# Kernel tuning notes

Measured on AMD Instinct MI355X. Metric: run time of the kernel, lower is better.

The kernel has to match this reference:

```python
import jax, jax.numpy as jnp
import numpy as np

D_MODEL = 512
N_HEADS = 8
D_K = D_MODEL // N_HEADS
D_DTW = 21


def setup_inputs() -> dict:
    key = jax.random.key(0)
    ks = jax.random.split(key, 16)
    bs, S = 16, 512
    def lin(k, fan_in, shape):
        return jax.random.uniform(k, shape, jnp.float32, -1.0, 1.0) / np.sqrt(fan_in)
    return {
        "Q": jax.random.normal(ks[0], (bs, S, D_MODEL), jnp.float32),
        "K": jax.random.normal(ks[1], (bs, S, D_MODEL), jnp.float32),
        "V": jax.random.normal(ks[2], (bs, S, D_MODEL), jnp.float32),
        "G": jax.random.normal(ks[3], (bs, S, D_MODEL), jnp.float32),
        "dtw_cost": jax.random.uniform(ks[4], (bs, D_DTW, S, S), jnp.float32),
        "Wq": lin(ks[5], D_MODEL, (D_MODEL, D_MODEL)), "bq": lin(ks[6], D_MODEL, (D_MODEL,)),
        "Wk": lin(ks[7], D_MODEL, (D_MODEL, D_MODEL)), "bk": lin(ks[8], D_MODEL, (D_MODEL,)),
        "Wv": lin(ks[9], D_MODEL, (D_MODEL, D_MODEL)), "bv": lin(ks[10], D_MODEL, (D_MODEL,)),
        "Wd": lin(ks[11], D_DTW, (N_HEADS, D_DTW)), "bd": lin(ks[12], D_DTW, (N_HEADS,)),
        "Wo": lin(ks[13], D_MODEL, (D_MODEL, D_MODEL)), "bo": lin(ks[14], D_MODEL, (D_MODEL,)),
    }


def reference(Q, K, V, G, dtw_cost, Wq, bq, Wk, bk, Wv, bv, Wd, bd, Wo, bo):
    bs, S, _ = Q.shape
    # QKV projections, split into heads: [bs, H, S, dk]
    def proj(x, W, b):
        y = x @ W.T + b
        return y.reshape(bs, S, N_HEADS, D_K).transpose(0, 2, 1, 3)
    q = proj(Q, Wq, bq)
    k = proj(K, Wk, bk)
    v = proj(V, Wv, bv)
    # scaled dot-product scores [bs, H, S, S]
    scores = jnp.einsum("bhqd,bhkd->bhqk", q, k) / np.sqrt(D_K).astype(np.float32)
    # DTW-cost bias: linear over the cost-channel dim (21 -> H), added per head
    bias = jnp.einsum("bcqk,hc->bhqk", dtw_cost, Wd) + bd[None, :, None, None]
    attn = jax.nn.softmax(scores + bias, axis=-1)
    out = jnp.einsum("bhqk,bhkd->bhqd", attn, v)  # [bs, H, S, dk]
    concat = out.transpose(0, 2, 1, 3).reshape(bs, S, D_MODEL)
    output = concat @ Wo.T + bo
    return (output, attn)
```

## Files before the change

kernel.cpp:

```cpp
#include <hip/hip_runtime.h>
#include <hip/hip_bf16.h>
#include <cstddef>
#include <cstdint>

#define BS   16
#define SLEN 512
#define DM   512
#define NH   8
#define DK   64
#define DC   21

typedef __attribute__((ext_vector_type(8))) short short8;
typedef __attribute__((ext_vector_type(4))) float f32x4;
typedef __attribute__((ext_vector_type(8))) _Float16 h16x8;
typedef _Float16 h16x4a __attribute__((ext_vector_type(4), may_alias));

__device__ inline unsigned pack_bf16(float a, float b) {
    unsigned ua = __builtin_bit_cast(unsigned, a);
    unsigned ub = __builtin_bit_cast(unsigned, b);
    ua = (ua + 0x7fffu + ((ua >> 16) & 1u)) >> 16;
    ub = (ub + 0x7fffu + ((ub >> 16) & 1u)) >> 16;
    return ua | (ub << 16);
}
__device__ inline unsigned cvt2(float a, float b) { return pack_bf16(a, b); }
__device__ inline ushort bf16_1(float a) { return (ushort)(pack_bf16(a, 0.f) & 0xffffu); }
__device__ inline unsigned pk_f16(float a, float b) {
    return __builtin_bit_cast(unsigned, __builtin_amdgcn_cvt_pkrtz(a, b));
}

__device__ __host__ inline size_t bias_chunk_base(int bh, int q16) {
    return 2 * (((size_t)bh * SLEN + (size_t)q16) * SLEN);
}

template<int MODE>
__global__ __launch_bounds__(256) void gemm_bf16(
    const void* __restrict__ Xv, const float* __restrict__ W,
    const float* __restrict__ bias, void* __restrict__ outv)
{
    __shared__ alignas(16) ushort Atile[64 * 64];
    __shared__ alignas(16) ushort Btile[128 * 64];

    const float*  Xf = (const float*)Xv;
    const ushort* Xb = (const ushort*)Xv;

    const int tid = threadIdx.x;
    const int wave = tid >> 6, lane = tid & 63;
    const int lq = lane & 15, lg = lane >> 4;
    const int wr = wave >> 1, wc = wave & 1;
    const int m0 = blockIdx.x * 64;
    const int n0 = blockIdx.y * 128;

    f32x4 acc[2][4];
#pragma unroll
    for (int i = 0; i < 2; ++i)
#pragma unroll
        for (int j = 0; j < 4; ++j) acc[i][j] = (f32x4){0.f, 0.f, 0.f, 0.f};

    float4 pa[2][2], pb[4][2];
    uint4  qa[2];

#define LOAD_A(K0)                                                              \
    if (MODE == 3) {                                                            \
        _Pragma("unroll")                                                       \
        for (int i = 0; i < 2; ++i) {                                           \
            const int P = tid + 256 * i;                                        \
            const int row = P >> 3, sl = P & 7;                                 \
            qa[i] = *(const uint4*)&Xb[(size_t)(m0 + row) * 512 + (K0) + sl * 8]; \
        }                                                                       \
    } else {                                                                    \
        _Pragma("unroll")                                                       \
        for (int i = 0; i < 2; ++i) {                                           \
            const int P = tid + 256 * i;                                        \
            const int row = P >> 3, cp = P & 7;                                 \
            const float4* s = (const float4*)&Xf[(size_t)(m0 + row) * 512 + (K0) + cp * 8]; \
            pa[i][0] = s[0]; pa[i][1] = s[1];                                   \
        }                                                                       \
    }
#define LOAD_B(K0)                                                              \
    _Pragma("unroll")                                                           \
    for (int i = 0; i < 4; ++i) {                                               \
        const int P = tid + 256 * i;                                            \
        const int row = P >> 3, cp = P & 7;                                     \
        const float4* s = (const float4*)&W[(size_t)(n0 + row) * 512 + (K0) + cp * 8]; \
        pb[i][0] = s[0]; pb[i][1] = s[1];                                       \
    }

    LOAD_A(0)
    LOAD_B(0)

    for (int it = 0; it < 8; ++it) {
        __syncthreads();
        if (MODE == 3) {
#pragma unroll
            for (int i = 0; i < 2; ++i) {
                const int P = tid + 256 * i;
                const int row = P >> 3, sl = P & 7;
                *(uint4*)((char*)Atile + row * 128 + 16 * (sl ^ (row & 7))) = qa[i];
            }
        } else {
#pragma unroll
            for (int i = 0; i < 2; ++i) {
                const int P = tid + 256 * i;
                const int row = P >> 3, cp = P & 7;
                uint4 w;
                w.x = cvt2(pa[i][0].x, pa[i][0].y);
                w.y = cvt2(pa[i][0].z, pa[i][0].w);
                w.z = cvt2(pa[i][1].x, pa[i][1].y);
                w.w = cvt2(pa[i][1].z, pa[i][1].w);
                *(uint4*)((char*)Atile + row * 128 + 16 * (cp ^ (row & 7))) = w;
            }
        }
#pragma unroll
        for (int i = 0; i < 4; ++i) {
            const int P = tid + 256 * i;
            const int row = P >> 3, cp = P & 7;
            uint4 w;
            w.x = cvt2(pb[i][0].x, pb[i][0].y);
            w.y = cvt2(pb[i][0].z, pb[i][0].w);
            w.z = cvt2(pb[i][1].x, pb[i][1].y);
            w.w = cvt2(pb[i][1].z, pb[i][1].w);
            *(uint4*)((char*)Btile + row * 128 + 16 * (cp ^ (row & 7))) = w;
        }
        __syncthreads();

        if (it < 7) {
            const int kn = (it + 1) * 64;
            LOAD_A(kn)
            LOAD_B(kn)
        }

        short8 af[2][2], bfr[4][2];
#pragma unroll
        for (int mi = 0; mi < 2; ++mi)
#pragma unroll
            for (int kh = 0; kh < 2; ++kh) {
                const int row = wr * 32 + mi * 16 + lq;
                af[mi][kh] = *(const short8*)((const char*)Atile + row * 128 +
                                              16 * ((kh * 4 + lg) ^ (row & 7)));
            }
#pragma unroll
        for (int ni = 0; ni < 4; ++ni)
#pragma unroll
            for (int kh = 0; kh < 2; ++kh) {
                const int row = wc * 64 + ni * 16 + lq;
                bfr[ni][kh] = *(const short8*)((const char*)Btile + row * 128 +
                                               16 * ((kh * 4 + lg) ^ (row & 7)));
            }
        __builtin_amdgcn_s_setprio(1);
#pragma unroll
        for (int kh = 0; kh < 2; ++kh)
#pragma unroll
            for (int mi = 0; mi < 2; ++mi)
#pragma unroll
                for (int ni = 0; ni < 4; ++ni)
                    acc[mi][ni] = __builtin_amdgcn_mfma_f32_16x16x32_bf16(
                        af[mi][kh], bfr[ni][kh], acc[mi][ni], 0, 0, 0);
        __builtin_amdgcn_s_setprio(0);
    }
#undef LOAD_A
#undef LOAD_B

    if (MODE == 3) {
        float* out = (float*)outv;
#pragma unroll
        for (int mi = 0; mi < 2; ++mi) {
            const int mb = m0 + wr * 32 + mi * 16 + lg * 4;
#pragma unroll
            for (int ni = 0; ni < 4; ++ni) {
                const int n = n0 + wc * 64 + ni * 16 + lq;
                const float bb = bias[n];
#pragma unroll
                for (int r = 0; r < 4; ++r)
                    out[(size_t)(mb + r) * 512 + n] = acc[mi][ni][r] + bb;
            }
        }
    } else if (MODE == 1) {
        ushort* out = (ushort*)outv;
#pragma unroll
        for (int mi = 0; mi < 2; ++mi) {
            const int mb = m0 + wr * 32 + mi * 16 + lg * 4;
#pragma unroll
            for (int ni = 0; ni < 4; ++ni) {
                const int n = n0 + wc * 64 + ni * 16 + lq;
                const int h = n >> 6, d = n & 63;
                const float bb = bias[n];
#pragma unroll
                for (int r = 0; r < 4; ++r) {
                    const int m = mb + r;
                    const int bidx = m >> 9, s = m & 511;
                    out[((size_t)(bidx * NH + h) * SLEN + s) * DK + d] =
                        bf16_1(acc[mi][ni][r] + bb);
                }
            }
        }
    } else {
        ushort* out = (ushort*)outv;
#pragma unroll
        for (int mi = 0; mi < 2; ++mi) {
            const int mb = m0 + wr * 32 + mi * 16 + lg * 4;
            const int bidx = mb >> 9, s0 = mb & 511;
#pragma unroll
            for (int ni = 0; ni < 4; ++ni) {
                const int n = n0 + wc * 64 + ni * 16 + lq;
                const int h = n >> 6, d = n & 63;
                const float bb = bias[n];
                uint2 pk;
                pk.x = pk_f16(acc[mi][ni][0] + bb, acc[mi][ni][1] + bb);
                pk.y = pk_f16(acc[mi][ni][2] + bb, acc[mi][ni][3] + bb);
                *(uint2*)&out[((size_t)(bidx * NH + h) * DK + d) * SLEN + s0] = pk;
            }
        }
    }
}

__global__ __launch_bounds__(512) void bias_kernel(
    const float* __restrict__ dtw, const float* __restrict__ Wd,
    const float* __restrict__ bd, _Float16* __restrict__ bias16)
{
    __shared__ float wdl[NH * DC];
    __shared__ float bdl[NH];
    const int k = threadIdx.x;
    const int q = blockIdx.x;
    const int b = blockIdx.y;
    if (k < NH * DC) wdl[k] = Wd[k];
    if (k < NH) bdl[k] = bd[k];
    __syncthreads();

    float acc[NH];
#pragma unroll
    for (int h = 0; h < NH; ++h) acc[h] = bdl[h];

    const float* p = dtw + ((size_t)b * DC * SLEN + q) * SLEN + k;
#pragma unroll
    for (int c = 0; c < DC; ++c) {
        const float x = p[(size_t)c * SLEN * SLEN];
#pragma unroll
        for (int h = 0; h < NH; ++h) acc[h] += x * wdl[h * DC + c];
    }
    const int q16 = q & ~15, ql = q & 15;
    const size_t seg = 1024 * (size_t)ql + 64 * (size_t)(k >> 5) + (k & 31);
#pragma unroll
    for (int h = 0; h < NH; ++h) {
        const size_t base = bias_chunk_base(b * NH + h, q16);
        bias16[base + seg] = (_Float16)acc[h];
    }
}

__global__ __launch_bounds__(256, 3) void attn_mfma(
    const ushort* __restrict__ qb, const ushort* __restrict__ kb,
    const ushort* __restrict__ vt, float* __restrict__ attn,
    ushort* __restrict__ concat)
{
    __shared__ alignas(16) ushort Pbuf[4][2][16][32];

    const int tid = threadIdx.x;
    const int wave = tid >> 6;
    const int lane = tid & 63;
    const int lq = lane & 15;
    const int lg = lane >> 4;

    const unsigned l = blockIdx.x;
    const int g  = (int)((l & 7) + 8 * (l >> 6));
    const int qt = (int)((l >> 3) & 7);
    const int h = g & 7, b = g >> 3;
    const int bh = b * NH + h;
    const int q0 = qt * 64 + wave * 16;

    const ushort* qptr = qb + ((size_t)bh * SLEN + q0) * DK;
    const ushort* kptr = kb + (size_t)bh * SLEN * DK;
    const ushort* vptr = vt + (size_t)bh * DK * SLEN;
    float* attn_b = attn + ((size_t)bh * SLEN + q0) * SLEN;
    const _Float16* bias_row =
        (const _Float16*)attn + bias_chunk_base(bh, q0) + 1024 * (size_t)lq;

    const short8 qf0 = *(const short8*)&qptr[(size_t)lq * DK + lg * 8];
    const short8 qf1 = *(const short8*)&qptr[(size_t)lq * DK + lg * 8 + 32];

    float sum = 0.f;
#pragma unroll 8
    for (int kt = 0; kt < 32; ++kt) {
        const short8 a0 = *(const short8*)&kptr[(size_t)(kt * 16 + lq) * DK + lg * 8];
        const short8 a1 = *(const short8*)&kptr[(size_t)(kt * 16 + lq) * DK + lg * 8 + 32];
        f32x4 c = {0.f, 0.f, 0.f, 0.f};
        c = __builtin_amdgcn_mfma_f32_16x16x32_bf16(a0, qf0, c, 0, 0, 0);
        c = __builtin_amdgcn_mfma_f32_16x16x32_bf16(a1, qf1, c, 0, 0, 0);
        const h16x4a b4 = *(const h16x4a*)&bias_row[64 * (kt >> 1) + 16 * (kt & 1) + 4 * lg];
        const float s0 = c[0] * 0.125f + (float)b4[0];
        const float s1 = c[1] * 0.125f + (float)b4[1];
        const float s2 = c[2] * 0.125f + (float)b4[2];
        const float s3 = c[3] * 0.125f + (float)b4[3];
        sum += (__expf(s0) + __expf(s1)) + (__expf(s2) + __expf(s3));
    }
    sum += __shfl_xor(sum, 16);
    sum += __shfl_xor(sum, 32);
    const float inv = 1.0f / sum;

    f32x4 oacc[4] = {{0.f,0.f,0.f,0.f},{0.f,0.f,0.f,0.f},{0.f,0.f,0.f,0.f},{0.f,0.f,0.f,0.f}};

#pragma unroll 2
    for (int c2 = 15; c2 >= 0; --c2) {
        f32x4 ev[2];
#pragma unroll
        for (int t = 0; t < 2; ++t) {
            const int kt = 2 * c2 + t;
            const short8 a0 = *(const short8*)&kptr[(size_t)(kt * 16 + lq) * DK + lg * 8];
            const short8 a1 = *(const short8*)&kptr[(size_t)(kt * 16 + lq) * DK + lg * 8 + 32];
            f32x4 c = {0.f, 0.f, 0.f, 0.f};
            c = __builtin_amdgcn_mfma_f32_16x16x32_bf16(a0, qf0, c, 0, 0, 0);
            c = __builtin_amdgcn_mfma_f32_16x16x32_bf16(a1, qf1, c, 0, 0, 0);
            const h16x4a b4 = *(const h16x4a*)&bias_row[64 * c2 + 16 * t + 4 * lg];
            ev[t][0] = __expf(c[0] * 0.125f + (float)b4[0]);
            ev[t][1] = __expf(c[1] * 0.125f + (float)b4[1]);
            ev[t][2] = __expf(c[2] * 0.125f + (float)b4[2]);
            ev[t][3] = __expf(c[3] * 0.125f + (float)b4[3]);
        }
#pragma unroll
        for (int t = 0; t < 2; ++t)
            *(f32x4*)&attn_b[(size_t)lq * SLEN + (2 * c2 + t) * 16 + lg * 4] = ev[t] * inv;

        char* pb = (char*)&Pbuf[wave][c2 & 1][0][0];
#pragma unroll
        for (int t = 0; t < 2; ++t) {
            uint2 pk;
            pk.x = pk_f16(ev[t][0], ev[t][1]);
            pk.y = pk_f16(ev[t][2], ev[t][3]);
            const int slot = (t * 2 + (lg >> 1)) ^ (lq & 3);
            *(uint2*)(pb + lq * 64 + slot * 16 + (lg & 1) * 8) = pk;
        }
        asm volatile("s_waitcnt lgkmcnt(0)" ::: "memory");

        const h16x8 pa = *(const h16x8*)(pb + lq * 64 + (lg ^ (lq & 3)) * 16);
        __builtin_amdgcn_s_setprio(1);
#pragma unroll
        for (int dt = 0; dt < 4; ++dt) {
            const h16x8 vb8 = *(const h16x8*)&vptr[(size_t)(dt * 16 + lq) * SLEN + c2 * 32 + lg * 8];
            oacc[dt] = __builtin_amdgcn_mfma_f32_16x16x32_f16(pa, vb8, oacc[dt], 0, 0, 0);
        }
        __builtin_amdgcn_s_setprio(0);
    }

    ushort* cbase = concat + ((size_t)(b * SLEN + q0)) * DM + h * 64;
#pragma unroll
    for (int r = 0; r < 4; ++r) {
        const float iv = __shfl(inv, lg * 4 + r);
#pragma unroll
        for (int dt = 0; dt < 4; ++dt) {
            cbase[(size_t)(lg * 4 + r) * DM + dt * 16 + lq] = bf16_1(oacc[dt][r] * iv);
        }
    }
}

extern "C" void kernel_launch(void* const* d_in, const int* in_sizes, int n_in,
                              void* d_out, int out_size, void* d_ws, size_t ws_size,
                              hipStream_t stream)
{
    const float* Q   = (const float*)d_in[0];
    const float* K   = (const float*)d_in[1];
    const float* V   = (const float*)d_in[2];
    const float* dtw = (const float*)d_in[4];
    const float* Wq  = (const float*)d_in[5];
    const float* bq  = (const float*)d_in[6];
    const float* Wk  = (const float*)d_in[7];
    const float* bk  = (const float*)d_in[8];
    const float* Wv  = (const float*)d_in[9];
    const float* bv  = (const float*)d_in[10];
    const float* Wd  = (const float*)d_in[11];
    const float* bd  = (const float*)d_in[12];
    const float* Wo  = (const float*)d_in[13];
    const float* bo  = (const float*)d_in[14];

    float* out  = (float*)d_out;
    float* attn = out + (size_t)BS * SLEN * DM;
    _Float16* bias16 = (_Float16*)attn;

    const size_t PHS = (size_t)BS * NH * SLEN * DK;
    ushort* qb = (ushort*)d_ws;
    ushort* kb = qb + PHS;
    ushort* vt = kb + PHS;
    ushort* cb = vt + PHS;

    const dim3 gemm_grid(128, 4);

    gemm_bf16<1><<<gemm_grid, 256, 0, stream>>>(Q, Wq, bq, qb);
    gemm_bf16<1><<<gemm_grid, 256, 0, stream>>>(K, Wk, bk, kb);
    gemm_bf16<2><<<gemm_grid, 256, 0, stream>>>(V, Wv, bv, vt);

    bias_kernel<<<dim3(SLEN, BS), 512, 0, stream>>>(dtw, Wd, bd, bias16);

    attn_mfma<<<dim3(1024), 256, 0, stream>>>(qb, kb, vt, attn, cb);

    gemm_bf16<3><<<gemm_grid, 256, 0, stream>>>(cb, Wo, bo, out);
}
```

Before: 299.6 us.

## Single-pass attention with deferred normalization; merge QKV GEMMs into one launch

The attention kernel no longer runs a separate QK^T and exp pass just to get the softmax denominator. It now computes scores once, writes unnormalized exp values to the attn output and accumulates the row sum. It then rescales the stored attn rows by 1/sum in a final read-modify-write loop. This removes half the score MFMAs and exps, but adds an extra read and write of the large attn tensor. The three QKV projection GEMMs are merged into one launch using blockIdx.z, the output GEMM gets its own kernel, the bias layout is regrouped to 32-wide chunks, and attention occupancy is raised to 4 blocks per CU.

```diff
diff --git a/kernel.cpp b/kernel.cpp
--- a/kernel.cpp
+++ b/kernel.cpp
@@ -32,16 +32,22 @@
     return 2 * (((size_t)bh * SLEN + (size_t)q16) * SLEN);
 }
 
-template<int MODE>
-__global__ __launch_bounds__(256) void gemm_bf16(
-    const void* __restrict__ Xv, const float* __restrict__ W,
-    const float* __restrict__ bias, void* __restrict__ outv)
+__global__ __launch_bounds__(256) void gemm_qkv(
+    const float* __restrict__ Q, const float* __restrict__ K,
+    const float* __restrict__ V,
+    const float* __restrict__ Wq, const float* __restrict__ Wk,
+    const float* __restrict__ Wv,
+    const float* __restrict__ bq, const float* __restrict__ bk,
+    const float* __restrict__ bv,
+    ushort* __restrict__ qb, ushort* __restrict__ kb, ushort* __restrict__ vt)
 {
     __shared__ alignas(16) ushort Atile[64 * 64];
     __shared__ alignas(16) ushort Btile[128 * 64];
 
-    const float*  Xf = (const float*)Xv;
-    const ushort* Xb = (const ushort*)Xv;
+    const int z = blockIdx.z;
+    const float* X    = (z == 0) ? Q  : (z == 1) ? K  : V;
+    const float* W    = (z == 0) ? Wq : (z == 1) ? Wk : Wv;
+    const float* bias = (z == 0) ? bq : (z == 1) ? bk : bv;
 
     const int tid = threadIdx.x;
     const int wave = tid >> 6, lane = tid & 63;
@@ -57,24 +63,14 @@
         for (int j = 0; j < 4; ++j) acc[i][j] = (f32x4){0.f, 0.f, 0.f, 0.f};
 
     float4 pa[2][2], pb[4][2];
-    uint4  qa[2];
 
 #define LOAD_A(K0)                                                              \
-    if (MODE == 3) {                                                            \
-        _Pragma("unroll")                                                       \
-        for (int i = 0; i < 2; ++i) {                                           \
-            const int P = tid + 256 * i;                                        \
-            const int row = P >> 3, sl = P & 7;                                 \
-            qa[i] = *(const uint4*)&Xb[(size_t)(m0 + row) * 512 + (K0) + sl * 8]; \
-        }                                                                       \
-    } else {                                                                    \
-        _Pragma("unroll")                                                       \
-        for (int i = 0; i < 2; ++i) {                                           \
-            const int P = tid + 256 * i;                                        \
-            const int row = P >> 3, cp = P & 7;                                 \
-            const float4* s = (const float4*)&Xf[(size_t)(m0 + row) * 512 + (K0) + cp * 8]; \
-            pa[i][0] = s[0]; pa[i][1] = s[1];                                   \
-        }                                                                       \
+    _Pragma("unroll")                                                           \
+    for (int i = 0; i < 2; ++i) {                                               \
+        const int P = tid + 256 * i;                                            \
+        const int row = P >> 3, cp = P & 7;                                     \
+        const float4* s = (const float4*)&X[(size_t)(m0 + row) * 512 + (K0) + cp * 8]; \
+        pa[i][0] = s[0]; pa[i][1] = s[1];                                       \
     }
 #define LOAD_B(K0)                                                              \
     _Pragma("unroll")                                                           \
@@ -90,25 +86,16 @@
 
     for (int it = 0; it < 8; ++it) {
         __syncthreads();
-        if (MODE == 3) {
-#pragma unroll
-            for (int i = 0; i < 2; ++i) {
-                const int P = tid + 256 * i;
-                const int row = P >> 3, sl = P & 7;
-                *(uint4*)((char*)Atile + row * 128 + 16 * (sl ^ (row & 7))) = qa[i];
-            }
-        } else {
-#pragma unroll
-            for (int i = 0; i < 2; ++i) {
-                const int P = tid + 256 * i;
-                const int row = P >> 3, cp = P & 7;
-                uint4 w;
-                w.x = cvt2(pa[i][0].x, pa[i][0].y);
-                w.y = cvt2(pa[i][0].z, pa[i][0].w);
-                w.z = cvt2(pa[i][1].x, pa[i][1].y);
-                w.w = cvt2(pa[i][1].z, pa[i][1].w);
-                *(uint4*)((char*)Atile + row * 128 + 16 * (cp ^ (row & 7))) = w;
-            }
+#pragma unroll
+        for (int i = 0; i < 2; ++i) {
+            const int P = tid + 256 * i;
+            const int row = P >> 3, cp = P & 7;
+            uint4 w;
+            w.x = cvt2(pa[i][0].x, pa[i][0].y);
+            w.y = cvt2(pa[i][0].z, pa[i][0].w);
+            w.z = cvt2(pa[i][1].x, pa[i][1].y);
+            w.w = cvt2(pa[i][1].z, pa[i][1].w);
+            *(uint4*)((char*)Atile + row * 128 + 16 * (cp ^ (row & 7))) = w;
         }
 #pragma unroll
         for (int i = 0; i < 4; ++i) {
@@ -160,22 +147,8 @@
 #undef LOAD_A
 #undef LOAD_B
 
-    if (MODE == 3) {
-        float* out = (float*)outv;
-#pragma unroll
-        for (int mi = 0; mi < 2; ++mi) {
-            const int mb = m0 + wr * 32 + mi * 16 + lg * 4;
-#pragma unroll
-            for (int ni = 0; ni < 4; ++ni) {
-                const int n = n0 + wc * 64 + ni * 16 + lq;
-                const float bb = bias[n];
-#pragma unroll
-                for (int r = 0; r < 4; ++r)
-                    out[(size_t)(mb + r) * 512 + n] = acc[mi][ni][r] + bb;
-            }
-        }
-    } else if (MODE == 1) {
-        ushort* out = (ushort*)outv;
+    if (z < 2) {
+        ushort* out = (z == 0) ? qb : kb;
 #pragma unroll
         for (int mi = 0; mi < 2; ++mi) {
             const int mb = m0 + wr * 32 + mi * 16 + lg * 4;
@@ -194,7 +167,6 @@
             }
         }
     } else {
-        ushort* out = (ushort*)outv;
 #pragma unroll
         for (int mi = 0; mi < 2; ++mi) {
             const int mb = m0 + wr * 32 + mi * 16 + lg * 4;
@@ -207,8 +179,122 @@
                 uint2 pk;
                 pk.x = pk_f16(acc[mi][ni][0] + bb, acc[mi][ni][1] + bb);
                 pk.y = pk_f16(acc[mi][ni][2] + bb, acc[mi][ni][3] + bb);
-                *(uint2*)&out[((size_t)(bidx * NH + h) * DK + d) * SLEN + s0] = pk;
-            }
+                *(uint2*)&vt[((size_t)(bidx * NH + h) * DK + d) * SLEN + s0] = pk;
+            }
+        }
+    }
+}
+
+__global__ __launch_bounds__(256) void gemm_out(
+    const ushort* __restrict__ Xb, const float* __restrict__ W,
+    const float* __restrict__ bias, float* __restrict__ out)
+{
+    __shared__ alignas(16) ushort Atile[64 * 64];
+    __shared__ alignas(16) ushort Btile[128 * 64];
+
+    const int tid = threadIdx.x;
+    const int wave = tid >> 6, lane = tid & 63;
+    const int lq = lane & 15, lg = lane >> 4;
+    const int wr = wave >> 1, wc = wave & 1;
+    const int m0 = blockIdx.x * 64;
+    const int n0 = blockIdx.y * 128;
+
+    f32x4 acc[2][4];
+#pragma unroll
+    for (int i = 0; i < 2; ++i)
+#pragma unroll
+        for (int j = 0; j < 4; ++j) acc[i][j] = (f32x4){0.f, 0.f, 0.f, 0.f};
+
+    uint4  qa[2];
+    float4 pb[4][2];
+
+#define LOAD_A(K0)                                                              \
+    _Pragma("unroll")                                                           \
+    for (int i = 0; i < 2; ++i) {                                               \
+        const int P = tid + 256 * i;                                            \
+        const int row = P >> 3, sl = P & 7;                                     \
+        qa[i] = *(const uint4*)&Xb[(size_t)(m0 + row) * 512 + (K0) + sl * 8];   \
+    }
+#define LOAD_B(K0)                                                              \
+    _Pragma("unroll")                                                           \
+    for (int i = 0; i < 4; ++i) {                                               \
+        const int P = tid + 256 * i;                                            \
+        const int row = P >> 3, cp = P & 7;                                     \
+        const float4* s = (const float4*)&W[(size_t)(n0 + row) * 512 + (K0) + cp * 8]; \
+        pb[i][0] = s[0]; pb[i][1] = s[1];                                       \
+    }
+
+    LOAD_A(0)
+    LOAD_B(0)
+
+    for (int it = 0; it < 8; ++it) {
+        __syncthreads();
+#pragma unroll
+        for (int i = 0; i < 2; ++i) {
+            const int P = tid + 256 * i;
+            const int row = P >> 3, sl = P & 7;
+            *(uint4*)((char*)Atile + row * 128 + 16 * (sl ^ (row & 7))) = qa[i];
+        }
+#pragma unroll
+        for (int i = 0; i < 4; ++i) {
+            const int P = tid + 256 * i;
+            const int row = P >> 3, cp = P & 7;
+            uint4 w;
+            w.x = cvt2(pb[i][0].x, pb[i][0].y);
+            w.y = cvt2(pb[i][0].z, pb[i][0].w);
+            w.z = cvt2(pb[i][1].x, pb[i][1].y);
+            w.w = cvt2(pb[i][1].z, pb[i][1].w);
+            *(uint4*)((char*)Btile + row * 128 + 16 * (cp ^ (row & 7))) = w;
+        }
+        __syncthreads();
+
+        if (it < 7) {
+            const int kn = (it + 1) * 64;
+            LOAD_A(kn)
+            LOAD_B(kn)
+        }
+
+        short8 af[2][2], bfr[4][2];
+#pragma unroll
+        for (int mi = 0; mi < 2; ++mi)
+#pragma unroll
+            for (int kh = 0; kh < 2; ++kh) {
+                const int row = wr * 32 + mi * 16 + lq;
+                af[mi][kh] = *(const short8*)((const char*)Atile + row * 128 +
+                                              16 * ((kh * 4 + lg) ^ (row & 7)));
+            }
+#pragma unroll
+        for (int ni = 0; ni < 4; ++ni)
+#pragma unroll
+            for (int kh = 0; kh < 2; ++kh) {
+                const int row = wc * 64 + ni * 16 + lq;
+                bfr[ni][kh] = *(const short8*)((const char*)Btile + row * 128 +
+                                               16 * ((kh * 4 + lg) ^ (row & 7)));
+            }
+        __builtin_amdgcn_s_setprio(1);
+#pragma unroll
+        for (int kh = 0; kh < 2; ++kh)
+#pragma unroll
+            for (int mi = 0; mi < 2; ++mi)
+#pragma unroll
+                for (int ni = 0; ni < 4; ++ni)
+                    acc[mi][ni] = __builtin_amdgcn_mfma_f32_16x16x32_bf16(
+                        af[mi][kh], bfr[ni][kh], acc[mi][ni], 0, 0, 0);
+        __builtin_amdgcn_s_setprio(0);
+    }
+#undef LOAD_A
+#undef LOAD_B
+
+#pragma unroll
+    for (int mi = 0; mi < 2; ++mi) {
+        const int mb = m0 + wr * 32 + mi * 16 + lg * 4;
+#pragma unroll
+        for (int ni = 0; ni < 4; ++ni) {
+            const int n = n0 + wc * 64 + ni * 16 + lq;
+            const float bb = bias[n];
+#pragma unroll
+            for (int r = 0; r < 4; ++r)
+                out[(size_t)(mb + r) * 512 + n] = acc[mi][ni][r] + bb;
         }
     }
 }
@@ -238,7 +324,7 @@
         for (int h = 0; h < NH; ++h) acc[h] += x * wdl[h * DC + c];
     }
     const int q16 = q & ~15, ql = q & 15;
-    const size_t seg = 1024 * (size_t)ql + 64 * (size_t)(k >> 5) + (k & 31);
+    const size_t seg = 1024 * (size_t)ql + 32 * (size_t)(k >> 4) + (k & 15);
 #pragma unroll
     for (int h = 0; h < NH; ++h) {
         const size_t base = bias_chunk_base(b * NH + h, q16);
@@ -246,7 +332,7 @@
     }
 }
 
-__global__ __launch_bounds__(256, 3) void attn_mfma(
+__global__ __launch_bounds__(256, 4) void attn_mfma(
     const ushort* __restrict__ qb, const ushort* __restrict__ kb,
     const ushort* __restrict__ vt, float* __restrict__ attn,
     ushort* __restrict__ concat)
@@ -277,29 +363,10 @@
     const short8 qf1 = *(const short8*)&qptr[(size_t)lq * DK + lg * 8 + 32];
 
     float sum = 0.f;
-#pragma unroll 8
-    for (int kt = 0; kt < 32; ++kt) {
-        const short8 a0 = *(const short8*)&kptr[(size_t)(kt * 16 + lq) * DK + lg * 8];
-        const short8 a1 = *(const short8*)&kptr[(size_t)(kt * 16 + lq) * DK + lg * 8 + 32];
-        f32x4 c = {0.f, 0.f, 0.f, 0.f};
-        c = __builtin_amdgcn_mfma_f32_16x16x32_bf16(a0, qf0, c, 0, 0, 0);
-        c = __builtin_amdgcn_mfma_f32_16x16x32_bf16(a1, qf1, c, 0, 0, 0);
-        const h16x4a b4 = *(const h16x4a*)&bias_row[64 * (kt >> 1) + 16 * (kt & 1) + 4 * lg];
-        const float s0 = c[0] * 0.125f + (float)b4[0];
-        const float s1 = c[1] * 0.125f + (float)b4[1];
-        const float s2 = c[2] * 0.125f + (float)b4[2];
-        const float s3 = c[3] * 0.125f + (float)b4[3];
-        sum += (__expf(s0) + __expf(s1)) + (__expf(s2) + __expf(s3));
-    }
-    sum += __shfl_xor(sum, 16);
-    sum += __shfl_xor(sum, 32);
-    const float inv = 1.0f / sum;
-
     f32x4 oacc[4] = {{0.f,0.f,0.f,0.f},{0.f,0.f,0.f,0.f},{0.f,0.f,0.f,0.f},{0.f,0.f,0.f,0.f}};
 
-#pragma unroll 2
-    for (int c2 = 15; c2 >= 0; --c2) {
-        f32x4 ev[2];
+    for (int c2 = 0; c2 < 16; ++c2) {
+        char* pb = (char*)&Pbuf[wave][c2 & 1][0][0];
 #pragma unroll
         for (int t = 0; t < 2; ++t) {
             const int kt = 2 * c2 + t;
@@ -308,22 +375,17 @@
             f32x4 c = {0.f, 0.f, 0.f, 0.f};
             c = __builtin_amdgcn_mfma_f32_16x16x32_bf16(a0, qf0, c, 0, 0, 0);
             c = __builtin_amdgcn_mfma_f32_16x16x32_bf16(a1, qf1, c, 0, 0, 0);
-            const h16x4a b4 = *(const h16x4a*)&bias_row[64 * c2 + 16 * t + 4 * lg];
-            ev[t][0] = __expf(c[0] * 0.125f + (float)b4[0]);
-            ev[t][1] = __expf(c[1] * 0.125f + (float)b4[1]);
-            ev[t][2] = __expf(c[2] * 0.125f + (float)b4[2]);
-            ev[t][3] = __expf(c[3] * 0.125f + (float)b4[3]);
-        }
-#pragma unroll
-        for (int t = 0; t < 2; ++t)
-            *(f32x4*)&attn_b[(size_t)lq * SLEN + (2 * c2 + t) * 16 + lg * 4] = ev[t] * inv;
-
-        char* pb = (char*)&Pbuf[wave][c2 & 1][0][0];
-#pragma unroll
-        for (int t = 0; t < 2; ++t) {
+            const h16x4a b4 = *(const h16x4a*)&bias_row[32 * kt + 4 * lg];
+            f32x4 e;
+            e[0] = __expf(c[0] * 0.125f + (float)b4[0]);
+            e[1] = __expf(c[1] * 0.125f + (float)b4[1]);
+            e[2] = __expf(c[2] * 0.125f + (float)b4[2]);
+            e[3] = __expf(c[3] * 0.125f + (float)b4[3]);
+            sum += (e[0] + e[1]) + (e[2] + e[3]);
+            *(f32x4*)&attn_b[(size_t)lq * SLEN + kt * 16 + lg * 4] = e;
             uint2 pk;
-            pk.x = pk_f16(ev[t][0], ev[t][1]);
-            pk.y = pk_f16(ev[t][2], ev[t][3]);
+            pk.x = pk_f16(e[0], e[1]);
+            pk.y = pk_f16(e[2], e[3]);
             const int slot = (t * 2 + (lg >> 1)) ^ (lq & 3);
             *(uint2*)(pb + lq * 64 + slot * 16 + (lg & 1) * 8) = pk;
         }
@@ -337,6 +399,18 @@
             oacc[dt] = __builtin_amdgcn_mfma_f32_16x16x32_f16(pa, vb8, oacc[dt], 0, 0, 0);
         }
         __builtin_amdgcn_s_setprio(0);
+    }
+
+    sum += __shfl_xor(sum, 16);
+    sum += __shfl_xor(sum, 32);
+    const float inv = 1.0f / sum;
+
+    asm volatile("s_waitcnt vmcnt(0)" ::: "memory");
+#pragma unroll 8
+    for (int i = 0; i < 32; ++i) {
+        float* p = &attn_b[(size_t)lq * SLEN + i * 16 + lg * 4];
+        f32x4 v = *(f32x4*)p;
+        *(f32x4*)p = v * inv;
     }
 
     ushort* cbase = concat + ((size_t)(b * SLEN + q0)) * DM + h * 64;
@@ -379,15 +453,12 @@
     ushort* vt = kb + PHS;
     ushort* cb = vt + PHS;
 
-    const dim3 gemm_grid(128, 4);
-
-    gemm_bf16<1><<<gemm_grid, 256, 0, stream>>>(Q, Wq, bq, qb);
-    gemm_bf16<1><<<gemm_grid, 256, 0, stream>>>(K, Wk, bk, kb);
-    gemm_bf16<2><<<gemm_grid, 256, 0, stream>>>(V, Wv, bv, vt);
+    gemm_qkv<<<dim3(128, 4, 3), 256, 0, stream>>>(Q, K, V, Wq, Wk, Wv,
+                                                  bq, bk, bv, qb, kb, vt);
 
     bias_kernel<<<dim3(SLEN, BS), 512, 0, stream>>>(dtw, Wd, bd, bias16);
 
     attn_mfma<<<dim3(1024), 256, 0, stream>>>(qb, kb, vt, attn, cb);
 
-    gemm_bf16<3><<<gemm_grid, 256, 0, stream>>>(cb, Wo, bo, out);
-}
+    gemm_out<<<dim3(128, 4), 256, 0, stream>>>(cb, Wo, bo, out);
+}
```

Result: slower. 318.1 us (+6.2%).

## Cache unnormalized fp16 exponentials in registers to skip the second QK pass

Applied to the files above, without the earlier changes.

The first pass now keeps the exponentiated scores packed as fp16 in a 32-entry register array, so the second pass no longer recomputes the QK MFMAs, bias loads and exps. The bias staging layout becomes plain row-major per 16-query chunk, and the second loop runs forward and fully unrolled. This removes half of the score MFMA and transcendental work but adds about 64 VGPRs per thread, which could cut occupancy under launch_bounds(256,3) or cause spills. The stored attn values are now rounded through fp16 before normalization, which slightly reduces their precision.

```diff
diff --git a/kernel.cpp b/kernel.cpp
--- a/kernel.cpp
+++ b/kernel.cpp
@@ -13,6 +13,8 @@
 typedef __attribute__((ext_vector_type(8))) short short8;
 typedef __attribute__((ext_vector_type(4))) float f32x4;
 typedef __attribute__((ext_vector_type(8))) _Float16 h16x8;
+typedef __attribute__((ext_vector_type(4))) _Float16 h16x4;
+typedef __attribute__((ext_vector_type(2))) unsigned u32x2;
 typedef _Float16 h16x4a __attribute__((ext_vector_type(4), may_alias));
 
 __device__ inline unsigned pack_bf16(float a, float b) {
@@ -238,11 +240,10 @@
         for (int h = 0; h < NH; ++h) acc[h] += x * wdl[h * DC + c];
     }
     const int q16 = q & ~15, ql = q & 15;
-    const size_t seg = 1024 * (size_t)ql + 64 * (size_t)(k >> 5) + (k & 31);
 #pragma unroll
     for (int h = 0; h < NH; ++h) {
         const size_t base = bias_chunk_base(b * NH + h, q16);
-        bias16[base + seg] = (_Float16)acc[h];
+        bias16[base + (size_t)ql * SLEN + k] = (_Float16)acc[h];
     }
 }
 
@@ -271,25 +272,31 @@
     const ushort* vptr = vt + (size_t)bh * DK * SLEN;
     float* attn_b = attn + ((size_t)bh * SLEN + q0) * SLEN;
     const _Float16* bias_row =
-        (const _Float16*)attn + bias_chunk_base(bh, q0) + 1024 * (size_t)lq;
+        (const _Float16*)attn + bias_chunk_base(bh, q0) + (size_t)lq * SLEN;
 
     const short8 qf0 = *(const short8*)&qptr[(size_t)lq * DK + lg * 8];
     const short8 qf1 = *(const short8*)&qptr[(size_t)lq * DK + lg * 8 + 32];
 
     float sum = 0.f;
-#pragma unroll 8
+    u32x2 ep[32];
+
+#pragma unroll
     for (int kt = 0; kt < 32; ++kt) {
         const short8 a0 = *(const short8*)&kptr[(size_t)(kt * 16 + lq) * DK + lg * 8];
         const short8 a1 = *(const short8*)&kptr[(size_t)(kt * 16 + lq) * DK + lg * 8 + 32];
         f32x4 c = {0.f, 0.f, 0.f, 0.f};
         c = __builtin_amdgcn_mfma_f32_16x16x32_bf16(a0, qf0, c, 0, 0, 0);
         c = __builtin_amdgcn_mfma_f32_16x16x32_bf16(a1, qf1, c, 0, 0, 0);
-        const h16x4a b4 = *(const h16x4a*)&bias_row[64 * (kt >> 1) + 16 * (kt & 1) + 4 * lg];
-        const float s0 = c[0] * 0.125f + (float)b4[0];
-        const float s1 = c[1] * 0.125f + (float)b4[1];
-        const float s2 = c[2] * 0.125f + (float)b4[2];
-        const float s3 = c[3] * 0.125f + (float)b4[3];
-        sum += (__expf(s0) + __expf(s1)) + (__expf(s2) + __expf(s3));
+        const h16x4a b4 = *(const h16x4a*)&bias_row[kt * 16 + 4 * lg];
+        const float e0 = __expf(c[0] * 0.125f + (float)b4[0]);
+        const float e1 = __expf(c[1] * 0.125f + (float)b4[1]);
+        const float e2 = __expf(c[2] * 0.125f + (float)b4[2]);
+        const float e3 = __expf(c[3] * 0.125f + (float)b4[3]);
+        sum += (e0 + e1) + (e2 + e3);
+        u32x2 pk;
+        pk[0] = pk_f16(e0, e1);
+        pk[1] = pk_f16(e2, e3);
+        ep[kt] = pk;
     }
     sum += __shfl_xor(sum, 16);
     sum += __shfl_xor(sum, 32);
@@ -297,35 +304,21 @@
 
     f32x4 oacc[4] = {{0.f,0.f,0.f,0.f},{0.f,0.f,0.f,0.f},{0.f,0.f,0.f,0.f},{0.f,0.f,0.f,0.f}};
 
-#pragma unroll 2
-    for (int c2 = 15; c2 >= 0; --c2) {
-        f32x4 ev[2];
+#pragma unroll
+    for (int c2 = 0; c2 < 16; ++c2) {
+        char* pb = (char*)&Pbuf[wave][c2 & 1][0][0];
 #pragma unroll
         for (int t = 0; t < 2; ++t) {
             const int kt = 2 * c2 + t;
-            const short8 a0 = *(const short8*)&kptr[(size_t)(kt * 16 + lq) * DK + lg * 8];
-            const short8 a1 = *(const short8*)&kptr[(size_t)(kt * 16 + lq) * DK + lg * 8 + 32];
-            f32x4 c = {0.f, 0.f, 0.f, 0.f};
-            c = __builtin_amdgcn_mfma_f32_16x16x32_bf16(a0, qf0, c, 0, 0, 0);
-            c = __builtin_amdgcn_mfma_f32_16x16x32_bf16(a1, qf1, c, 0, 0, 0);
-            const h16x4a b4 = *(const h16x4a*)&bias_row[64 * c2 + 16 * t + 4 * lg];
-            ev[t][0] = __expf(c[0] * 0.125f + (float)b4[0]);
-            ev[t][1] = __expf(c[1] * 0.125f + (float)b4[1]);
-            ev[t][2] = __expf(c[2] * 0.125f + (float)b4[2]);
-            ev[t][3] = __expf(c[3] * 0.125f + (float)b4[3]);
-        }
-#pragma unroll
-        for (int t = 0; t < 2; ++t)
-            *(f32x4*)&attn_b[(size_t)lq * SLEN + (2 * c2 + t) * 16 + lg * 4] = ev[t] * inv;
-
-        char* pb = (char*)&Pbuf[wave][c2 & 1][0][0];
-#pragma unroll
-        for (int t = 0; t < 2; ++t) {
-            uint2 pk;
-            pk.x = pk_f16(ev[t][0], ev[t][1]);
-            pk.y = pk_f16(ev[t][2], ev[t][3]);
+            const h16x4 hv = __builtin_bit_cast(h16x4, ep[kt]);
+            f32x4 a;
+            a[0] = (float)hv[0] * inv;
+            a[1] = (float)hv[1] * inv;
+            a[2] = (float)hv[2] * inv;
+            a[3] = (float)hv[3] * inv;
+            *(f32x4*)&attn_b[(size_t)lq * SLEN + kt * 16 + lg * 4] = a;
             const int slot = (t * 2 + (lg >> 1)) ^ (lq & 3);
-            *(uint2*)(pb + lq * 64 + slot * 16 + (lg & 1) * 8) = pk;
+            *(u32x2*)(pb + lq * 64 + slot * 16 + (lg & 1) * 8) = ep[kt];
         }
         asm volatile("s_waitcnt lgkmcnt(0)" ::: "memory");
 
```

Measured after the change: 253.2 us. 15.5% less time.
